# Optimization experiments

Measured on AMD Instinct MI355X. Metric: run time of the kernel, lower is better.

Reference implementation:

```python
import jax, jax.numpy as jnp
import numpy as np
from jax.scipy.special import logsumexp

B, T, D, K, H, A, EH = 256, 4096, 3, 2, 2, 5, 8


def setup_inputs() -> dict:
    key = jax.random.key(0)
    ks = jax.random.split(key, 14)
    p = lambda k, shape: jax.random.normal(k, shape, jnp.float32) * 0.1
    return {
        "x": jax.random.normal(ks[0], (B, T, D), jnp.float32),
        "Q_seq": jax.random.normal(ks[1], (B, T, A, 2), jnp.float32),
        "log_pi": p(ks[2], (K,)),
        "log_A": p(ks[3], (K, K)),
        "fc1_w": p(ks[4], (EH, D)),
        "fc1_b": p(ks[5], (EH,)),
        "fc2_w": p(ks[6], (K, EH)),
        "fc2_b": p(ks[7], (K,)),
        "w_ih": p(ks[8], (3 * H, D)),
        "w_hh": p(ks[9], (3 * H, H)),
        "b_ih": p(ks[10], (3 * H,)),
        "b_hh": p(ks[11], (3 * H,)),
        "Wg": p(ks[12], (K, H, A)),
        "by": p(ks[13], (K, 2)),
    }


def reference(x, Q_seq, log_pi, log_A, fc1_w, fc1_b, fc2_w, fc2_b,
              w_ih, w_hh, b_ih, b_hh, Wg, by):
    Bn, Tn, _ = x.shape
    Hn = w_hh.shape[1]

    # ---- GRU (torch semantics: r,z,n gate order) ----
    def gru_step(h, xt):
        gi = xt @ w_ih.T + b_ih            # [B,3H]
        gh = h @ w_hh.T + b_hh
        ir, iz, inn = jnp.split(gi, 3, axis=-1)
        hr, hz, hn = jnp.split(gh, 3, axis=-1)
        r = jax.nn.sigmoid(ir + hr)
        z = jax.nn.sigmoid(iz + hz)
        n = jnp.tanh(inn + r * hn)
        h_new = (1.0 - z) * n + z * h
        return h_new, h_new

    xs = jnp.swapaxes(x, 0, 1)             # [T,B,D]
    _, hs = jax.lax.scan(gru_step, jnp.zeros((Bn, Hn), x.dtype), xs)
    h = jnp.swapaxes(hs, 0, 1)             # [B,T,H]

    # ---- Phase emitter ----
    e = jax.nn.log_softmax(jnp.tanh(x @ fc1_w.T + fc1_b) @ fc2_w.T + fc2_b, axis=-1)  # [B,T,K]

    # ---- HMM forward-backward ----
    lpi = jax.nn.log_softmax(log_pi)
    lA = jax.nn.log_softmax(log_A, axis=1)
    eT = jnp.swapaxes(e, 0, 1)             # [T,B,K]

    a0 = lpi + eT[0]
    def astep(a, et):
        an = logsumexp(a[:, :, None] + lA[None], axis=1) + et
        return an, an
    _, arest = jax.lax.scan(astep, a0, eT[1:])
    alpha = jnp.concatenate([a0[None], arest], axis=0)   # [T,B,K]

    bN = jnp.zeros_like(a0)
    def bstep(b, et1):
        bt = logsumexp(b[:, None, :] + lA[None] + et1[:, None, :], axis=2)
        return bt, bt
    _, brest = jax.lax.scan(bstep, bN, eT[1:], reverse=True)
    beta = jnp.concatenate([brest, bN[None]], axis=0)    # [T,B,K]

    lg = alpha + beta
    lg = lg - logsumexp(lg, axis=-1, keepdims=True)
    log_gamma = jnp.swapaxes(lg, 0, 1)     # [B,T,K]
    gamma = jnp.exp(log_gamma)

    # ---- Mixture-of-agents gating ----
    Wh = jnp.einsum('bth,kha->btka', h, Wg)
    gk = jax.nn.softmax(Wh, axis=-1)
    g = jnp.einsum('btk,btka->bta', gamma, gk)
    V = jnp.einsum('bta,btay->bty', g, Q_seq) + jnp.einsum('btk,kc->btc', gamma, by)
    pi_log = jax.nn.log_softmax(V, axis=-1)
    return pi_log, g, log_gamma
```

## Files before the change

### kernel.cpp

```cpp
#include <hip/hip_runtime.h>
#include <math.h>

constexpr int Bn = 256;
constexpr int Tn = 4096;
constexpr int BT = Bn * Tn;

constexpr int CG  = 64,  WGu = 64;
constexpr int CAc = 128;
constexpr int CBc = 128;
constexpr int NGRU = (Tn / CG)  * (Bn / 64);
constexpr int NALP = (Tn / CAc) * (Bn / 64);
constexpr int NBET = (Tn / CBc) * (Bn / 64);

__device__ __forceinline__ float sigp(float x) {
  float x2 = x * x;
  float p = fmaf(x2, 2.0833333e-3f, -2.0833333e-2f);
  p = fmaf(x2, p, 0.25f);
  return fmaf(x, p, 0.5f);
}
__device__ __forceinline__ float tanhp(float x) {
  float x2 = x * x;
  float num = fmaf(x2, x2 + 105.0f, 945.0f);
  float den = fmaf(x2, fmaf(x2, 15.0f, 420.0f), 945.0f);
  return x * num * __builtin_amdgcn_rcpf(den);
}

__global__ __launch_bounds__(256) void k1_pre(
    const float* __restrict__ x,
    const float* __restrict__ fc1_w, const float* __restrict__ fc1_b,
    const float* __restrict__ fc2_w, const float* __restrict__ fc2_b,
    const float* __restrict__ w_ih,  const float* __restrict__ b_ih,
    const float* __restrict__ b_hh,
    float4* __restrict__ grz, float2* __restrict__ gn, float2* __restrict__ E)
{
  int idx = blockIdx.x * 256 + threadIdx.x;
  float x0 = x[3 * idx + 0], x1 = x[3 * idx + 1], x2 = x[3 * idx + 2];

  float4 gv;
  gv.x = fmaf(x2, w_ih[2],  fmaf(x1, w_ih[1],  fmaf(x0, w_ih[0],  b_ih[0] + b_hh[0])));
  gv.y = fmaf(x2, w_ih[5],  fmaf(x1, w_ih[4],  fmaf(x0, w_ih[3],  b_ih[1] + b_hh[1])));
  gv.z = fmaf(x2, w_ih[8],  fmaf(x1, w_ih[7],  fmaf(x0, w_ih[6],  b_ih[2] + b_hh[2])));
  gv.w = fmaf(x2, w_ih[11], fmaf(x1, w_ih[10], fmaf(x0, w_ih[9],  b_ih[3] + b_hh[3])));
  float2 nv;
  nv.x = fmaf(x2, w_ih[14], fmaf(x1, w_ih[13], fmaf(x0, w_ih[12], b_ih[4])));
  nv.y = fmaf(x2, w_ih[17], fmaf(x1, w_ih[16], fmaf(x0, w_ih[15], b_ih[5])));
  grz[idx] = gv;
  gn[idx] = nv;

  float zk0 = fc2_b[0], zk1 = fc2_b[1];
#pragma unroll
  for (int u = 0; u < 8; ++u) {
    float a = fmaf(x2, fc1_w[u * 3 + 2], fmaf(x1, fc1_w[u * 3 + 1], fmaf(x0, fc1_w[u * 3 + 0], fc1_b[u])));
    float e2 = __expf(2.0f * a);
    float th = 1.0f - 2.0f * __builtin_amdgcn_rcpf(1.0f + e2);
    zk0 = fmaf(th, fc2_w[u], zk0);
    zk1 = fmaf(th, fc2_w[8 + u], zk1);
  }
  float m = fmaxf(zk0, zk1);
  E[idx] = make_float2(__expf(zk0 - m), __expf(zk1 - m));
}

#define GRU_LOAD(BG, BN, S0) \
  { _Pragma("unroll") for (int i = 0; i < 8; ++i) { BG[i] = gp[(S0) + i]; BN[i] = np[(S0) + i]; } }

#define GRU_GROUP(BG, BN, S0, ST) \
  { _Pragma("unroll") for (int i = 0; i < 8; ++i) { \
      float4 g4 = BG[i]; float2 g2 = BN[i]; \
      float pr0 = fmaf(h1, W01, fmaf(h0, W00, g4.x)); \
      float pr1 = fmaf(h1, W11, fmaf(h0, W10, g4.y)); \
      float pz0 = fmaf(h1, W21, fmaf(h0, W20, g4.z)); \
      float pz1 = fmaf(h1, W31, fmaf(h0, W30, g4.w)); \
      float hn0 = fmaf(h1, W41, fmaf(h0, W40, B4)); \
      float hn1 = fmaf(h1, W51, fmaf(h0, W50, B5)); \
      float r0 = sigp(pr0), r1 = sigp(pr1); \
      float z0 = sigp(pz0), z1 = sigp(pz1); \
      float n0 = tanhp(fmaf(r0, hn0, g2.x)); \
      float n1 = tanhp(fmaf(r1, hn1, g2.y)); \
      h0 = fmaf(z0, h0 - n0, n0); \
      h1 = fmaf(z1, h1 - n1, n1); \
      if (ST) hp[(S0) + i] = make_float2(h0, h1); \
  } }

#define ALP_LOAD(BUF, TB) \
  { _Pragma("unroll") for (int i = 0; i < 16; ++i) { BUF[i] = Ep[(TB) + i]; } }

#define ALP_GROUP(BUF, TB, ST, SK) \
  { _Pragma("unroll") for (int i = 0; i < 16; ++i) { \
      float2 e2 = BUF[i]; \
      if (!((SK) && i == 0)) { \
        float an0 = fmaf(a1, A10, a0 * A00) * e2.x; \
        float an1 = fmaf(a1, A11, a0 * A01) * e2.y; \
        a0 = an0; a1 = an1; } \
      if (ST) ap[(TB) + i] = make_float2(a0, a1); \
    } \
    float rs = __builtin_amdgcn_rcpf(a0 + a1); a0 *= rs; a1 *= rs; }

#define BET_LOAD(BUF, TB, CL) \
  { _Pragma("unroll") for (int i = 0; i < 16; ++i) { \
      int li = (TB) + 1 - i; if ((CL) && i == 0) li = Tn - 1; \
      BUF[i] = Ep[li]; } }

#define BET_GROUP(BUF, TB, ST, SK) \
  { _Pragma("unroll") for (int i = 0; i < 16; ++i) { \
      float2 e2 = BUF[i]; \
      if (!((SK) && i == 0)) { \
        float f0 = e2.x * bb0, f1 = e2.y * bb1; \
        float nb0 = fmaf(A01, f1, A00 * f0); \
        float nb1 = fmaf(A11, f1, A10 * f0); \
        bb0 = nb0; bb1 = nb1; } \
      if (ST) bp[(TB) - i] = make_float2(bb0, bb1); \
    } \
    float rs = __builtin_amdgcn_rcpf(bb0 + bb1); bb0 *= rs; bb1 *= rs; }

__global__ __launch_bounds__(64) void k2_scan(
    const float4* __restrict__ grz, const float2* __restrict__ gn,
    const float2* __restrict__ E,
    float2* __restrict__ h, float2* __restrict__ alpha, float2* __restrict__ beta,
    const float* __restrict__ w_hh, const float* __restrict__ b_hh,
    const float* __restrict__ log_pi, const float* __restrict__ log_A)
{
  int blk = blockIdx.x;
  int lane = threadIdx.x;

  if (blk < NGRU) {
    int c = blk >> 2;
    int b = ((blk & 3) << 6) + lane;
    int t0 = c * CG;
    int tstart = (c == 0) ? 0 : (t0 - WGu);
    int ng = (t0 + CG - tstart) >> 3;
    int wg = (t0 - tstart) >> 3;
    const float4* gp = grz + (size_t)b * Tn + tstart;
    const float2* np = gn + (size_t)b * Tn + tstart;
    float2* hp = h + (size_t)b * Tn + tstart;

    float W00 = w_hh[0], W01 = w_hh[1], W10 = w_hh[2],  W11 = w_hh[3];
    float W20 = w_hh[4], W21 = w_hh[5], W30 = w_hh[6],  W31 = w_hh[7];
    float W40 = w_hh[8], W41 = w_hh[9], W50 = w_hh[10], W51 = w_hh[11];
    float B4 = b_hh[4], B5 = b_hh[5];

    float h0 = 0.f, h1 = 0.f;
    float4 AG[8], BG[8];
    float2 AN[8], BN[8];
    GRU_LOAD(AG, AN, 0);
    GRU_LOAD(BG, BN, 8);
    for (int g = 0; g < ng; g += 2) {
      bool stA = g >= wg;
      GRU_GROUP(AG, AN, g * 8, stA);
      if (g + 2 < ng) GRU_LOAD(AG, AN, (g + 2) * 8);
      bool stB = (g + 1) >= wg;
      GRU_GROUP(BG, BN, (g + 1) * 8, stB);
      if (g + 3 < ng) GRU_LOAD(BG, BN, (g + 3) * 8);
    }
  } else if (blk < NGRU + NALP) {
    int bk = blk - NGRU;
    int c = bk >> 2;
    int b = ((bk & 3) << 6) + lane;
    int t0 = c * CAc;
    const float2* Ep = E + (size_t)b * Tn;
    float2* ap = alpha + (size_t)b * Tn;

    float la0 = log_A[0], la1 = log_A[1], la2 = log_A[2], la3 = log_A[3];
    float m0 = fmaxf(la0, la1), m1 = fmaxf(la2, la3);
    float e00 = __expf(la0 - m0), e01 = __expf(la1 - m0);
    float e10 = __expf(la2 - m1), e11 = __expf(la3 - m1);
    float i0 = 1.0f / (e00 + e01), i1 = 1.0f / (e10 + e11);
    float A00 = e00 * i0, A01 = e01 * i0, A10 = e10 * i1, A11 = e11 * i1;

    float a0, a1;
    int tlo, ngroups, sg;
    bool skip0;
    if (c == 0) {
      float p0 = log_pi[0], p1 = log_pi[1];
      float mp = fmaxf(p0, p1);
      float2 E0 = Ep[0];
      a0 = __expf(p0 - mp) * E0.x;
      a1 = __expf(p1 - mp) * E0.y;
      tlo = 0; ngroups = CAc / 16; sg = 0; skip0 = true;
    } else {
      a0 = 1.f; a1 = 1.f;
      tlo = t0 - 32; ngroups = (CAc + 32) / 16; sg = 2; skip0 = false;
    }

    float2 EA[16], EB[16];
    ALP_LOAD(EA, tlo);
    ALP_LOAD(EB, tlo + 16);
    for (int g = 0; g < ngroups; g += 2) {
      { bool st = g >= sg; bool sk = skip0 && (g == 0);
        ALP_GROUP(EA, tlo + g * 16, st, sk); }
      if (g + 2 < ngroups) ALP_LOAD(EA, tlo + (g + 2) * 16);
      { bool st = (g + 1) >= sg;
        ALP_GROUP(EB, tlo + (g + 1) * 16, st, false); }
      if (g + 3 < ngroups) ALP_LOAD(EB, tlo + (g + 3) * 16);
    }
  } else {
    int bk = blk - NGRU - NALP;
    int c = bk >> 2;
    int b = ((bk & 3) << 6) + lane;
    int t0 = c * CBc;
    int t1 = t0 + CBc - 1;
    const float2* Ep = E + (size_t)b * Tn;
    float2* bp = beta + (size_t)b * Tn;

    float la0 = log_A[0], la1 = log_A[1], la2 = log_A[2], la3 = log_A[3];
    float m0 = fmaxf(la0, la1), m1 = fmaxf(la2, la3);
    float e00 = __expf(la0 - m0), e01 = __expf(la1 - m0);
    float e10 = __expf(la2 - m1), e11 = __expf(la3 - m1);
    float i0 = 1.0f / (e00 + e01), i1 = 1.0f / (e10 + e11);
    float A00 = e00 * i0, A01 = e01 * i0, A10 = e10 * i1, A11 = e11 * i1;

    float bb0 = 1.f, bb1 = 1.f;
    int thi, ngroups, sg;
    bool skip0, cl0;
    if (t1 == Tn - 1) {
      thi = t1; ngroups = CBc / 16; sg = 0; skip0 = true; cl0 = true;
    } else {
      thi = t1 + 32; ngroups = (CBc + 32) / 16; sg = 2; skip0 = false; cl0 = false;
    }

    float2 FA[16], FB[16];
    BET_LOAD(FA, thi, cl0);
    BET_LOAD(FB, thi - 16, false);
    for (int g = 0; g < ngroups; g += 2) {
      { bool st = g >= sg; bool sk = skip0 && (g == 0);
        BET_GROUP(FA, thi - g * 16, st, sk); }
      if (g + 2 < ngroups) BET_LOAD(FA, thi - (g + 2) * 16, false);
      { bool st = (g + 1) >= sg;
        BET_GROUP(FB, thi - (g + 1) * 16, st, false); }
      if (g + 3 < ngroups) BET_LOAD(FB, thi - (g + 3) * 16, false);
    }
  }
}

__global__ __launch_bounds__(256) void k3_out(
    const float2* __restrict__ h, const float2* __restrict__ alpha,
    const float2* __restrict__ beta, const float* __restrict__ Q,
    const float* __restrict__ Wg, const float* __restrict__ by,
    float* __restrict__ out_pi, float* __restrict__ out_g, float* __restrict__ out_lg)
{
  int idx = blockIdx.x * 256 + threadIdx.x;
  float2 hv = h[idx], av = alpha[idx], bv = beta[idx];

  float p0 = av.x * bv.x, p1 = av.y * bv.y;
  float invs = 1.0f / (p0 + p1);
  float gamma0 = p0 * invs, gamma1 = p1 * invs;
  float lg0 = __logf(gamma0), lg1 = __logf(gamma1);

  float wh0[5], wh1[5];
#pragma unroll
  for (int a = 0; a < 5; ++a) {
    wh0[a] = fmaf(hv.y, Wg[5 + a],  hv.x * Wg[a]);
    wh1[a] = fmaf(hv.y, Wg[15 + a], hv.x * Wg[10 + a]);
  }
  float mx0 = wh0[0], mx1 = wh1[0];
#pragma unroll
  for (int a = 1; a < 5; ++a) { mx0 = fmaxf(mx0, wh0[a]); mx1 = fmaxf(mx1, wh1[a]); }
  float ex0[5], ex1[5];
  float s0 = 0.f, s1 = 0.f;
#pragma unroll
  for (int a = 0; a < 5; ++a) {
    ex0[a] = __expf(wh0[a] - mx0); s0 += ex0[a];
    ex1[a] = __expf(wh1[a] - mx1); s1 += ex1[a];
  }
  float r0 = 1.0f / s0, r1 = 1.0f / s1;
  float c0 = gamma0 * r0, c1 = gamma1 * r1;

  const float2* q2 = (const float2*)(Q + (size_t)idx * 10);
  float2 qv[5];
#pragma unroll
  for (int a = 0; a < 5; ++a) qv[a] = q2[a];

  float V0 = fmaf(gamma1, by[2], gamma0 * by[0]);
  float V1 = fmaf(gamma1, by[3], gamma0 * by[1]);
  float ga[5];
#pragma unroll
  for (int a = 0; a < 5; ++a) {
    ga[a] = fmaf(c1, ex1[a], c0 * ex0[a]);
    V0 = fmaf(ga[a], qv[a].x, V0);
    V1 = fmaf(ga[a], qv[a].y, V1);
  }
#pragma unroll
  for (int a = 0; a < 5; ++a) out_g[(size_t)idx * 5 + a] = ga[a];

  float mv = fmaxf(V0, V1);
  float l = mv + __logf(__expf(V0 - mv) + __expf(V1 - mv));
  ((float2*)out_pi)[idx] = make_float2(V0 - l, V1 - l);
  ((float2*)out_lg)[idx] = make_float2(lg0, lg1);
}

extern "C" void kernel_launch(void* const* d_in, const int* in_sizes, int n_in,
                              void* d_out, int out_size, void* d_ws, size_t ws_size,
                              hipStream_t stream) {
  const float* x      = (const float*)d_in[0];
  const float* Q      = (const float*)d_in[1];
  const float* log_pi = (const float*)d_in[2];
  const float* log_A  = (const float*)d_in[3];
  const float* fc1_w  = (const float*)d_in[4];
  const float* fc1_b  = (const float*)d_in[5];
  const float* fc2_w  = (const float*)d_in[6];
  const float* fc2_b  = (const float*)d_in[7];
  const float* w_ih   = (const float*)d_in[8];
  const float* w_hh   = (const float*)d_in[9];
  const float* b_ih   = (const float*)d_in[10];
  const float* b_hh   = (const float*)d_in[11];
  const float* Wg     = (const float*)d_in[12];
  const float* by     = (const float*)d_in[13];

  float* ws = (float*)d_ws;
  float4* grz   = (float4*)ws;
  float2* gn    = (float2*)(ws + (size_t)4 * BT);
  float2* E     = (float2*)(ws + (size_t)6 * BT);
  float2* h     = (float2*)(ws + (size_t)8 * BT);
  float2* alpha = (float2*)(ws + (size_t)10 * BT);
  float2* beta  = (float2*)(ws + (size_t)12 * BT);
  float* out = (float*)d_out;

  k1_pre<<<BT / 256, 256, 0, stream>>>(x, fc1_w, fc1_b, fc2_w, fc2_b, w_ih, b_ih, b_hh, grz, gn, E);
  k2_scan<<<NGRU + NALP + NBET, 64, 0, stream>>>(grz, gn, E, h, alpha, beta, w_hh, b_hh, log_pi, log_A);
  k3_out<<<BT / 256, 256, 0, stream>>>(h, alpha, beta, Q, Wg, by,
                                       out, out + (size_t)2 * BT, out + (size_t)7 * BT);
}
```

Before: 160.6 us.

## Store intermediates as fp16 in time-major layout with LDS transposes

All workspace intermediates (gate preactivations, emissions, h, alpha, beta) are stored as half2 instead of float and transposed to [T,B] layout, so the per-batch scan threads read coalesced rows. The pre and output kernels gain a 16x16 shared-memory transpose to convert between the [B,T] input/output layout and the time-major workspace. The GRU math is repacked into float2 operations, and alpha/beta renormalization now happens every 8 steps. The aim is to halve workspace traffic and get coalesced scan accesses. In exchange it adds fp16 rounding error to the recurrences and stored probabilities.

```diff
diff --git a/kernel.cpp b/kernel.cpp
--- a/kernel.cpp
+++ b/kernel.cpp
@@ -1,28 +1,40 @@
 #include <hip/hip_runtime.h>
+#include <hip/hip_fp16.h>
 #include <math.h>
 
 constexpr int Bn = 256;
 constexpr int Tn = 4096;
 constexpr int BT = Bn * Tn;
 
-constexpr int CG  = 64,  WGu = 64;
+constexpr int CG  = 64;
 constexpr int CAc = 128;
 constexpr int CBc = 128;
 constexpr int NGRU = (Tn / CG)  * (Bn / 64);
 constexpr int NALP = (Tn / CAc) * (Bn / 64);
 constexpr int NBET = (Tn / CBc) * (Bn / 64);
 
-__device__ __forceinline__ float sigp(float x) {
-  float x2 = x * x;
-  float p = fmaf(x2, 2.0833333e-3f, -2.0833333e-2f);
-  p = fmaf(x2, p, 0.25f);
-  return fmaf(x, p, 0.5f);
-}
-__device__ __forceinline__ float tanhp(float x) {
-  float x2 = x * x;
-  float num = fmaf(x2, x2 + 105.0f, 945.0f);
-  float den = fmaf(x2, fmaf(x2, 15.0f, 420.0f), 945.0f);
-  return x * num * __builtin_amdgcn_rcpf(den);
+struct __align__(8) h4 { __half2 x, y; };
+
+__device__ __forceinline__ float2 f2(float a, float b){ return make_float2(a,b); }
+__device__ __forceinline__ float2 f2s(float a){ return make_float2(a,a); }
+__device__ __forceinline__ float2 f2add(float2 a, float2 b){ return f2(a.x+b.x, a.y+b.y); }
+__device__ __forceinline__ float2 f2sub(float2 a, float2 b){ return f2(a.x-b.x, a.y-b.y); }
+__device__ __forceinline__ float2 f2mul(float2 a, float2 b){ return f2(a.x*b.x, a.y*b.y); }
+__device__ __forceinline__ float2 f2fma(float2 a, float2 b, float2 c){
+  return f2(fmaf(a.x,b.x,c.x), fmaf(a.y,b.y,c.y)); }
+
+__device__ __forceinline__ float2 sigp2(float2 x) {
+  float2 x2 = f2mul(x, x);
+  float2 p = f2fma(x2, f2s(2.0833333e-3f), f2s(-2.0833333e-2f));
+  p = f2fma(x2, p, f2s(0.25f));
+  return f2fma(x, p, f2s(0.5f));
+}
+__device__ __forceinline__ float2 tanhp2(float2 x) {
+  float2 x2 = f2mul(x, x);
+  float2 num = f2fma(x2, f2add(x2, f2s(105.f)), f2s(945.f));
+  float2 den = f2fma(x2, f2fma(x2, f2s(15.f), f2s(420.f)), f2s(945.f));
+  return f2(x.x * num.x * __builtin_amdgcn_rcpf(den.x),
+            x.y * num.y * __builtin_amdgcn_rcpf(den.y));
 }
 
 __global__ __launch_bounds__(256) void k1_pre(
@@ -31,91 +43,106 @@
     const float* __restrict__ fc2_w, const float* __restrict__ fc2_b,
     const float* __restrict__ w_ih,  const float* __restrict__ b_ih,
     const float* __restrict__ b_hh,
-    float4* __restrict__ grz, float2* __restrict__ gn, float2* __restrict__ E)
+    h4* __restrict__ grz, __half2* __restrict__ gn, __half2* __restrict__ E)
 {
-  int idx = blockIdx.x * 256 + threadIdx.x;
-  float x0 = x[3 * idx + 0], x1 = x[3 * idx + 1], x2 = x[3 * idx + 2];
-
-  float4 gv;
-  gv.x = fmaf(x2, w_ih[2],  fmaf(x1, w_ih[1],  fmaf(x0, w_ih[0],  b_ih[0] + b_hh[0])));
-  gv.y = fmaf(x2, w_ih[5],  fmaf(x1, w_ih[4],  fmaf(x0, w_ih[3],  b_ih[1] + b_hh[1])));
-  gv.z = fmaf(x2, w_ih[8],  fmaf(x1, w_ih[7],  fmaf(x0, w_ih[6],  b_ih[2] + b_hh[2])));
-  gv.w = fmaf(x2, w_ih[11], fmaf(x1, w_ih[10], fmaf(x0, w_ih[9],  b_ih[3] + b_hh[3])));
-  float2 nv;
-  nv.x = fmaf(x2, w_ih[14], fmaf(x1, w_ih[13], fmaf(x0, w_ih[12], b_ih[4])));
-  nv.y = fmaf(x2, w_ih[17], fmaf(x1, w_ih[16], fmaf(x0, w_ih[15], b_ih[5])));
-  grz[idx] = gv;
-  gn[idx] = nv;
-
-  float zk0 = fc2_b[0], zk1 = fc2_b[1];
-#pragma unroll
-  for (int u = 0; u < 8; ++u) {
-    float a = fmaf(x2, fc1_w[u * 3 + 2], fmaf(x1, fc1_w[u * 3 + 1], fmaf(x0, fc1_w[u * 3 + 0], fc1_b[u])));
-    float e2 = __expf(2.0f * a);
-    float th = 1.0f - 2.0f * __builtin_amdgcn_rcpf(1.0f + e2);
-    zk0 = fmaf(th, fc2_w[u], zk0);
-    zk1 = fmaf(th, fc2_w[8 + u], zk1);
-  }
-  float m = fmaxf(zk0, zk1);
-  E[idx] = make_float2(__expf(zk0 - m), __expf(zk1 - m));
-}
-
-#define GRU_LOAD(BG, BN, S0) \
-  { _Pragma("unroll") for (int i = 0; i < 8; ++i) { BG[i] = gp[(S0) + i]; BN[i] = np[(S0) + i]; } }
-
-#define GRU_GROUP(BG, BN, S0, ST) \
+  __shared__ h4      Lg[16][17];
+  __shared__ __half2 Ln[16][17];
+  __shared__ __half2 LE[16][17];
+  int tid = threadIdx.x;
+  int btile = blockIdx.x >> 8;
+  int ttile = blockIdx.x & 255;
+
+  {
+    int bl = tid >> 4, tl = tid & 15;
+    int b = btile * 16 + bl, t = ttile * 16 + tl;
+    const float* xp = x + ((size_t)b * Tn + t) * 3;
+    float x0 = xp[0], x1 = xp[1], x2 = xp[2];
+
+    float gr0 = fmaf(x2, w_ih[2],  fmaf(x1, w_ih[1],  fmaf(x0, w_ih[0],  b_ih[0] + b_hh[0])));
+    float gr1 = fmaf(x2, w_ih[5],  fmaf(x1, w_ih[4],  fmaf(x0, w_ih[3],  b_ih[1] + b_hh[1])));
+    float gz0 = fmaf(x2, w_ih[8],  fmaf(x1, w_ih[7],  fmaf(x0, w_ih[6],  b_ih[2] + b_hh[2])));
+    float gz1 = fmaf(x2, w_ih[11], fmaf(x1, w_ih[10], fmaf(x0, w_ih[9],  b_ih[3] + b_hh[3])));
+    float gn0 = fmaf(x2, w_ih[14], fmaf(x1, w_ih[13], fmaf(x0, w_ih[12], b_ih[4])));
+    float gn1 = fmaf(x2, w_ih[17], fmaf(x1, w_ih[16], fmaf(x0, w_ih[15], b_ih[5])));
+
+    float zk0 = fc2_b[0], zk1 = fc2_b[1];
+#pragma unroll
+    for (int u = 0; u < 8; ++u) {
+      float a = fmaf(x2, fc1_w[u*3+2], fmaf(x1, fc1_w[u*3+1], fmaf(x0, fc1_w[u*3+0], fc1_b[u])));
+      float e2 = __expf(2.0f * a);
+      float th = 1.0f - 2.0f * __builtin_amdgcn_rcpf(1.0f + e2);
+      zk0 = fmaf(th, fc2_w[u], zk0);
+      zk1 = fmaf(th, fc2_w[8 + u], zk1);
+    }
+    float m = fmaxf(zk0, zk1);
+    h4 g; g.x = __float22half2_rn(f2(gr0, gr1)); g.y = __float22half2_rn(f2(gz0, gz1));
+    Lg[tl][bl] = g;
+    Ln[tl][bl] = __float22half2_rn(f2(gn0, gn1));
+    LE[tl][bl] = __float22half2_rn(f2(__expf(zk0 - m), __expf(zk1 - m)));
+  }
+  __syncthreads();
+  {
+    int tl = tid >> 4, bl = tid & 15;
+    int b = btile * 16 + bl, t = ttile * 16 + tl;
+    size_t o = (size_t)t * Bn + b;
+    grz[o] = Lg[tl][bl];
+    gn[o]  = Ln[tl][bl];
+    E[o]   = LE[tl][bl];
+  }
+}
+
+#define GRU_LOAD(BG, BN_, S0) \
   { _Pragma("unroll") for (int i = 0; i < 8; ++i) { \
-      float4 g4 = BG[i]; float2 g2 = BN[i]; \
-      float pr0 = fmaf(h1, W01, fmaf(h0, W00, g4.x)); \
-      float pr1 = fmaf(h1, W11, fmaf(h0, W10, g4.y)); \
-      float pz0 = fmaf(h1, W21, fmaf(h0, W20, g4.z)); \
-      float pz1 = fmaf(h1, W31, fmaf(h0, W30, g4.w)); \
-      float hn0 = fmaf(h1, W41, fmaf(h0, W40, B4)); \
-      float hn1 = fmaf(h1, W51, fmaf(h0, W50, B5)); \
-      float r0 = sigp(pr0), r1 = sigp(pr1); \
-      float z0 = sigp(pz0), z1 = sigp(pz1); \
-      float n0 = tanhp(fmaf(r0, hn0, g2.x)); \
-      float n1 = tanhp(fmaf(r1, hn1, g2.y)); \
-      h0 = fmaf(z0, h0 - n0, n0); \
-      h1 = fmaf(z1, h1 - n1, n1); \
-      if (ST) hp[(S0) + i] = make_float2(h0, h1); \
+      BG[i] = gp[(size_t)((S0) + i) * Bn]; BN_[i] = np[(size_t)((S0) + i) * Bn]; } }
+
+#define GRU_GROUP(BG, BN_, S0, ST) \
+  { _Pragma("unroll") for (int i = 0; i < 8; ++i) { \
+      float2 gA = __half22float2(BG[i].x); \
+      float2 gB = __half22float2(BG[i].y); \
+      float2 gN = __half22float2(BN_[i]); \
+      float2 h00 = f2s(hv.x), h11 = f2s(hv.y); \
+      float2 pr = f2fma(h00, Wr0, f2fma(h11, Wr1, gA)); \
+      float2 pz = f2fma(h00, Wz0, f2fma(h11, Wz1, gB)); \
+      float2 hn = f2fma(h00, Wn0, f2fma(h11, Wn1, Bn2)); \
+      float2 r = sigp2(pr), z = sigp2(pz); \
+      float2 n = tanhp2(f2fma(r, hn, gN)); \
+      hv = f2fma(z, f2sub(hv, n), n); \
+      if (ST) hp[(size_t)((S0) + i) * Bn] = __float22half2_rn(hv); \
   } }
 
 #define ALP_LOAD(BUF, TB) \
-  { _Pragma("unroll") for (int i = 0; i < 16; ++i) { BUF[i] = Ep[(TB) + i]; } }
+  { _Pragma("unroll") for (int i = 0; i < 16; ++i) { BUF[i] = Ep[(size_t)((TB) + i) * Bn]; } }
 
 #define ALP_GROUP(BUF, TB, ST, SK) \
   { _Pragma("unroll") for (int i = 0; i < 16; ++i) { \
-      float2 e2 = BUF[i]; \
+      float2 e2 = __half22float2(BUF[i]); \
       if (!((SK) && i == 0)) { \
-        float an0 = fmaf(a1, A10, a0 * A00) * e2.x; \
-        float an1 = fmaf(a1, A11, a0 * A01) * e2.y; \
-        a0 = an0; a1 = an1; } \
-      if (ST) ap[(TB) + i] = make_float2(a0, a1); \
-    } \
-    float rs = __builtin_amdgcn_rcpf(a0 + a1); a0 *= rs; a1 *= rs; }
+        av = f2mul(f2fma(f2s(av.y), A1v, f2mul(f2s(av.x), A0v)), e2); } \
+      if (ST) ap[(size_t)((TB) + i) * Bn] = __float22half2_rn(av); \
+      if (i == 7 || i == 15) { \
+        float rs = __builtin_amdgcn_rcpf(av.x + av.y); av.x *= rs; av.y *= rs; } \
+  } }
 
 #define BET_LOAD(BUF, TB, CL) \
   { _Pragma("unroll") for (int i = 0; i < 16; ++i) { \
       int li = (TB) + 1 - i; if ((CL) && i == 0) li = Tn - 1; \
-      BUF[i] = Ep[li]; } }
+      BUF[i] = Ep[(size_t)li * Bn]; } }
 
 #define BET_GROUP(BUF, TB, ST, SK) \
   { _Pragma("unroll") for (int i = 0; i < 16; ++i) { \
-      float2 e2 = BUF[i]; \
+      float2 e2 = __half22float2(BUF[i]); \
       if (!((SK) && i == 0)) { \
-        float f0 = e2.x * bb0, f1 = e2.y * bb1; \
-        float nb0 = fmaf(A01, f1, A00 * f0); \
-        float nb1 = fmaf(A11, f1, A10 * f0); \
-        bb0 = nb0; bb1 = nb1; } \
-      if (ST) bp[(TB) - i] = make_float2(bb0, bb1); \
-    } \
-    float rs = __builtin_amdgcn_rcpf(bb0 + bb1); bb0 *= rs; bb1 *= rs; }
+        float2 f = f2mul(e2, bv); \
+        bv = f2fma(f2s(f.y), AB1, f2mul(f2s(f.x), AB0)); } \
+      if (ST) bp[(size_t)((TB) - i) * Bn] = __float22half2_rn(bv); \
+      if (i == 7 || i == 15) { \
+        float rs = __builtin_amdgcn_rcpf(bv.x + bv.y); bv.x *= rs; bv.y *= rs; } \
+  } }
 
 __global__ __launch_bounds__(64) void k2_scan(
-    const float4* __restrict__ grz, const float2* __restrict__ gn,
-    const float2* __restrict__ E,
-    float2* __restrict__ h, float2* __restrict__ alpha, float2* __restrict__ beta,
+    const h4* __restrict__ grz, const __half2* __restrict__ gn,
+    const __half2* __restrict__ E,
+    __half2* __restrict__ h, __half2* __restrict__ alpha, __half2* __restrict__ beta,
     const float* __restrict__ w_hh, const float* __restrict__ b_hh,
     const float* __restrict__ log_pi, const float* __restrict__ log_A)
 {
@@ -126,29 +153,27 @@
     int c = blk >> 2;
     int b = ((blk & 3) << 6) + lane;
     int t0 = c * CG;
-    int tstart = (c == 0) ? 0 : (t0 - WGu);
-    int ng = (t0 + CG - tstart) >> 3;
-    int wg = (t0 - tstart) >> 3;
-    const float4* gp = grz + (size_t)b * Tn + tstart;
-    const float2* np = gn + (size_t)b * Tn + tstart;
-    float2* hp = h + (size_t)b * Tn + tstart;
-
-    float W00 = w_hh[0], W01 = w_hh[1], W10 = w_hh[2],  W11 = w_hh[3];
-    float W20 = w_hh[4], W21 = w_hh[5], W30 = w_hh[6],  W31 = w_hh[7];
-    float W40 = w_hh[8], W41 = w_hh[9], W50 = w_hh[10], W51 = w_hh[11];
-    float B4 = b_hh[4], B5 = b_hh[5];
-
-    float h0 = 0.f, h1 = 0.f;
-    float4 AG[8], BG[8];
-    float2 AN[8], BN[8];
+    int tstart = (c == 0) ? 0 : (t0 - CG);
+    int ng = (c == 0) ? 8 : 16;
+    int wg = (c == 0) ? 0 : 8;
+    const h4*      gp = grz + (size_t)tstart * Bn + b;
+    const __half2* np = gn  + (size_t)tstart * Bn + b;
+    __half2*       hp = h   + (size_t)tstart * Bn + b;
+
+    float2 Wr0 = f2(w_hh[0], w_hh[2]), Wr1 = f2(w_hh[1], w_hh[3]);
+    float2 Wz0 = f2(w_hh[4], w_hh[6]), Wz1 = f2(w_hh[5], w_hh[7]);
+    float2 Wn0 = f2(w_hh[8], w_hh[10]), Wn1 = f2(w_hh[9], w_hh[11]);
+    float2 Bn2 = f2(b_hh[4], b_hh[5]);
+
+    float2 hv = f2s(0.f);
+    h4 AG[8], BG[8];
+    __half2 AN[8], BN[8];
     GRU_LOAD(AG, AN, 0);
     GRU_LOAD(BG, BN, 8);
     for (int g = 0; g < ng; g += 2) {
-      bool stA = g >= wg;
-      GRU_GROUP(AG, AN, g * 8, stA);
+      { bool st = g >= wg; GRU_GROUP(AG, AN, g * 8, st); }
       if (g + 2 < ng) GRU_LOAD(AG, AN, (g + 2) * 8);
-      bool stB = (g + 1) >= wg;
-      GRU_GROUP(BG, BN, (g + 1) * 8, stB);
+      { bool st = (g + 1) >= wg; GRU_GROUP(BG, BN, (g + 1) * 8, st); }
       if (g + 3 < ng) GRU_LOAD(BG, BN, (g + 3) * 8);
     }
   } else if (blk < NGRU + NALP) {
@@ -156,32 +181,32 @@
     int c = bk >> 2;
     int b = ((bk & 3) << 6) + lane;
     int t0 = c * CAc;
-    const float2* Ep = E + (size_t)b * Tn;
-    float2* ap = alpha + (size_t)b * Tn;
+    const __half2* Ep = E + b;
+    __half2* ap = alpha + b;
 
     float la0 = log_A[0], la1 = log_A[1], la2 = log_A[2], la3 = log_A[3];
     float m0 = fmaxf(la0, la1), m1 = fmaxf(la2, la3);
     float e00 = __expf(la0 - m0), e01 = __expf(la1 - m0);
     float e10 = __expf(la2 - m1), e11 = __expf(la3 - m1);
     float i0 = 1.0f / (e00 + e01), i1 = 1.0f / (e10 + e11);
-    float A00 = e00 * i0, A01 = e01 * i0, A10 = e10 * i1, A11 = e11 * i1;
-
-    float a0, a1;
+    float A00 = e00*i0, A01 = e01*i0, A10 = e10*i1, A11 = e11*i1;
+    float2 A0v = f2(A00, A01), A1v = f2(A10, A11);
+
+    float2 av;
     int tlo, ngroups, sg;
     bool skip0;
     if (c == 0) {
       float p0 = log_pi[0], p1 = log_pi[1];
       float mp = fmaxf(p0, p1);
-      float2 E0 = Ep[0];
-      a0 = __expf(p0 - mp) * E0.x;
-      a1 = __expf(p1 - mp) * E0.y;
+      float2 E0 = __half22float2(Ep[0]);
+      av = f2(__expf(p0 - mp) * E0.x, __expf(p1 - mp) * E0.y);
       tlo = 0; ngroups = CAc / 16; sg = 0; skip0 = true;
     } else {
-      a0 = 1.f; a1 = 1.f;
+      av = f2s(1.f);
       tlo = t0 - 32; ngroups = (CAc + 32) / 16; sg = 2; skip0 = false;
     }
 
-    float2 EA[16], EB[16];
+    __half2 EA[16], EB[16];
     ALP_LOAD(EA, tlo);
     ALP_LOAD(EB, tlo + 16);
     for (int g = 0; g < ngroups; g += 2) {
@@ -198,17 +223,18 @@
     int b = ((bk & 3) << 6) + lane;
     int t0 = c * CBc;
     int t1 = t0 + CBc - 1;
-    const float2* Ep = E + (size_t)b * Tn;
-    float2* bp = beta + (size_t)b * Tn;
+    const __half2* Ep = E + b;
+    __half2* bp = beta + b;
 
     float la0 = log_A[0], la1 = log_A[1], la2 = log_A[2], la3 = log_A[3];
     float m0 = fmaxf(la0, la1), m1 = fmaxf(la2, la3);
     float e00 = __expf(la0 - m0), e01 = __expf(la1 - m0);
     float e10 = __expf(la2 - m1), e11 = __expf(la3 - m1);
     float i0 = 1.0f / (e00 + e01), i1 = 1.0f / (e10 + e11);
-    float A00 = e00 * i0, A01 = e01 * i0, A10 = e10 * i1, A11 = e11 * i1;
-
-    float bb0 = 1.f, bb1 = 1.f;
+    float A00 = e00*i0, A01 = e01*i0, A10 = e10*i1, A11 = e11*i1;
+    float2 AB0 = f2(A00, A10), AB1 = f2(A01, A11);
+
+    float2 bv = f2s(1.f);
     int thi, ngroups, sg;
     bool skip0, cl0;
     if (t1 == Tn - 1) {
@@ -217,7 +243,7 @@
       thi = t1 + 32; ngroups = (CBc + 32) / 16; sg = 2; skip0 = false; cl0 = false;
     }
 
-    float2 FA[16], FB[16];
+    __half2 FA[16], FB[16];
     BET_LOAD(FA, thi, cl0);
     BET_LOAD(FB, thi - 16, false);
     for (int g = 0; g < ngroups; g += 2) {
@@ -232,13 +258,27 @@
 }
 
 __global__ __launch_bounds__(256) void k3_out(
-    const float2* __restrict__ h, const float2* __restrict__ alpha,
-    const float2* __restrict__ beta, const float* __restrict__ Q,
+    const __half2* __restrict__ h_, const __half2* __restrict__ a_,
+    const __half2* __restrict__ b_, const float* __restrict__ Q,
     const float* __restrict__ Wg, const float* __restrict__ by,
     float* __restrict__ out_pi, float* __restrict__ out_g, float* __restrict__ out_lg)
 {
-  int idx = blockIdx.x * 256 + threadIdx.x;
-  float2 hv = h[idx], av = alpha[idx], bv = beta[idx];
+  __shared__ __half2 Sh[16][17], Sa[16][17], Sb[16][17];
+  int tid = threadIdx.x;
+  int btile = blockIdx.x >> 8;
+  int ttile = blockIdx.x & 255;
+  {
+    int tl = tid >> 4, bl = tid & 15;
+    size_t o = (size_t)(ttile * 16 + tl) * Bn + btile * 16 + bl;
+    Sh[tl][bl] = h_[o]; Sa[tl][bl] = a_[o]; Sb[tl][bl] = b_[o];
+  }
+  __syncthreads();
+  int bl = tid >> 4, tl = tid & 15;
+  int b = btile * 16 + bl, t = ttile * 16 + tl;
+  size_t idx = (size_t)b * Tn + t;
+  float2 hv = __half22float2(Sh[tl][bl]);
+  float2 av = __half22float2(Sa[tl][bl]);
+  float2 bv = __half22float2(Sb[tl][bl]);
 
   float p0 = av.x * bv.x, p1 = av.y * bv.y;
   float invs = 1.0f / (p0 + p1);
@@ -264,7 +304,7 @@
   float r0 = 1.0f / s0, r1 = 1.0f / s1;
   float c0 = gamma0 * r0, c1 = gamma1 * r1;
 
-  const float2* q2 = (const float2*)(Q + (size_t)idx * 10);
+  const float2* q2 = (const float2*)(Q + idx * 10);
   float2 qv[5];
 #pragma unroll
   for (int a = 0; a < 5; ++a) qv[a] = q2[a];
@@ -279,7 +319,7 @@
     V1 = fmaf(ga[a], qv[a].y, V1);
   }
 #pragma unroll
-  for (int a = 0; a < 5; ++a) out_g[(size_t)idx * 5 + a] = ga[a];
+  for (int a = 0; a < 5; ++a) out_g[idx * 5 + a] = ga[a];
 
   float mv = fmaxf(V0, V1);
   float l = mv + __logf(__expf(V0 - mv) + __expf(V1 - mv));
@@ -305,13 +345,13 @@
   const float* Wg     = (const float*)d_in[12];
   const float* by     = (const float*)d_in[13];
 
-  float* ws = (float*)d_ws;
-  float4* grz   = (float4*)ws;
-  float2* gn    = (float2*)(ws + (size_t)4 * BT);
-  float2* E     = (float2*)(ws + (size_t)6 * BT);
-  float2* h     = (float2*)(ws + (size_t)8 * BT);
-  float2* alpha = (float2*)(ws + (size_t)10 * BT);
-  float2* beta  = (float2*)(ws + (size_t)12 * BT);
+  char* ws = (char*)d_ws;
+  h4*      grz   = (h4*)ws;
+  __half2* gn    = (__half2*)(ws + (size_t)8  * BT);
+  __half2* E     = (__half2*)(ws + (size_t)12 * BT);
+  __half2* h     = (__half2*)(ws + (size_t)16 * BT);
+  __half2* alpha = (__half2*)(ws + (size_t)20 * BT);
+  __half2* beta  = (__half2*)(ws + (size_t)24 * BT);
   float* out = (float*)d_out;
 
   k1_pre<<<BT / 256, 256, 0, stream>>>(x, fc1_w, fc1_b, fc2_w, fc2_b, w_ih, b_ih, b_hh, grz, gn, E);
```

Result: faster. 154.5 us (-3.8%).
